# Kernel tuning notes

Measured on AMD Instinct MI355X. Metric: run time of the kernel, lower is better.

Reference implementation:

```python
import jax, jax.numpy as jnp
import numpy as np

N = 50000   # nodes
E = 600000  # edges / hyperedge incidences
D = 128     # node_in_dim
H = 128     # hidden_dim
TAU = 0.5
ALPHA = 0.5
LAM = 0.5

_PARAM_SHAPES = [('Wq0', (1, H)), ('bq0', (H,)), ('W0', (D, H)), ('b0', (H,)),
                 ('Whq0', (1, H)), ('bhq0', (H,)), ('Wh0', (D, H)), ('bh0', (H,)),
                 ('Wf0', (H, H)), ('bf0', (H,)), ('Wfh0', (H, H)), ('bfh0', (H,)),
                 ('aq0', (H,)), ('a0', (H,)), ('ahq0', (H,)), ('ah0', (H,)),
                 ('aq_', (H,)), ('a_', (H,)), ('ahq_', (H,)), ('ah_', (H,)),
                 ('Wlq', (1, H)), ('blq', (H,)), ('Wlf', (D, H)), ('blf', (H,)),
                 ('Wm1', (H, H)), ('bm1', (H,)), ('Wm2', (H, H)), ('bm2', (H,))]


def setup_inputs() -> dict:
    key = jax.random.key(0)
    ks = jax.random.split(key, 8 + len(_PARAM_SHAPES))
    inp = {}
    inp['feats'] = jax.random.normal(ks[0], (N, D), dtype=jnp.float32)
    inp['edge_index'] = jax.random.randint(ks[1], (2, E), 0, N).astype(jnp.int32)
    inp['edge_index_aug'] = jax.random.randint(ks[2], (2, E), 0, N).astype(jnp.int32)
    inp['pos'] = jax.random.randint(ks[3], (100,), 1, N).astype(jnp.int32)
    inp['q'] = 0
    for i, (nm, sh) in enumerate(_PARAM_SHAPES):
        inp[nm] = jax.random.normal(ks[4 + i], sh, dtype=jnp.float32) * 0.05
    return inp


def _forward(feats, Wq0, bq0, W0, b0, Whq0, bhq0, Wh0, bh0, Wf0, bf0, Wfh0, bfh0,
             aq0, a0, ahq0, ah0, aq_, a_, ahq_, ah_, Wlq, blq, Wlf, blf,
             Wm1, bm1, Wm2, bm2, edge_index, edge_index_aug, q, pos):
    # ---- GCNConv (PyG default: add self-loops + symmetric normalization) ----
    sl = jnp.arange(N, dtype=edge_index.dtype)
    src = jnp.concatenate([edge_index[0], sl])
    dst = jnp.concatenate([edge_index[1], sl])
    deg = jax.ops.segment_sum(jnp.ones(src.shape[0], jnp.float32), dst, num_segments=N)
    dinv = jax.lax.rsqrt(deg)  # deg >= 1 thanks to self-loops
    enorm = dinv[src] * dinv[dst]

    def gcn(x, W, b):
        xw = x @ W
        return jax.ops.segment_sum(xw[src] * enorm[:, None], dst, num_segments=N) + b

    # ---- HypergraphConv (PyG, no attention): X' = D^-1 H B^-1 H^T X W ----
    node = edge_index_aug[0]
    he = edge_index_aug[1]
    Be = jax.ops.segment_sum(jnp.ones((E,), jnp.float32), he, num_segments=N)
    Dn = jax.ops.segment_sum(jnp.ones((E,), jnp.float32), node, num_segments=N)
    Binv = jnp.where(Be > 0, 1.0 / Be, 0.0)
    Dninv = jnp.where(Dn > 0, 1.0 / Dn, 0.0)

    def hg(x, W, b):
        xw = x @ W
        me = jax.ops.segment_sum(xw[node], he, num_segments=N) * Binv[:, None]
        return jax.ops.segment_sum(me[he], node, num_segments=N) * Dninv[:, None] + b

    # ---- attention-weighted fusion of two views (softmax over 2 logits) ----
    def fuse(a, b, wa, wb):
        att = jax.nn.softmax(jnp.stack([a @ wa, b @ wb], axis=1), axis=1)  # [N,2]
        return att[:, 0:1] * a + att[:, 1:2] * b

    querys = jnp.zeros((N, 1), jnp.float32).at[q].set(1.0)
    hq = jax.nn.relu(gcn(querys, Wq0, bq0))
    h = jax.nn.relu(gcn(feats, W0, b0))
    hf = fuse(hq, h, aq0, a0)
    h_augq = jax.nn.relu(hg(querys, Whq0, bhq0))
    h_aug = jax.nn.relu(hg(feats, Wh0, bh0))
    h_augf = fuse(h_augq, h_aug, ahq0, ah0)
    querys2 = querys @ Wlq + blq
    feats2 = feats @ Wlf + blf
    hf_ = fuse(querys2, feats2, aq_, a_)
    hf = jax.nn.relu(hf + gcn(hf_, Wf0, bf0))
    hfh_ = fuse(querys2, feats2, ahq_, ah_)
    h_augf = jax.nn.relu(h_augf + hg(hfh_, Wfh0, bfh0))

    def mlp(x):
        return jax.nn.relu(x @ Wm1 + bm1) @ Wm2 + bm2

    z = mlp(hf)
    z_aug = mlp(h_augf)

    # ---- Contra loss ----
    def expcos(v, M):
        num = M @ v
        den = jnp.maximum(jnp.linalg.norm(M, axis=1) * jnp.linalg.norm(v), 1e-8)
        return jnp.exp(num / den / TAU)

    sim1 = expcos(z[q], z)
    sim_aug1 = expcos(z_aug[q], z_aug)
    sim2 = expcos(z[q], z_aug)
    sim_aug2 = expcos(z_aug[q], z)
    mask = jnp.zeros((N,), bool).at[pos].set(True).at[q].set(False)
    nmask = jnp.sum(mask).astype(jnp.float32)

    def nlm(s):  # mean over positives of -log(s_i / sum(s))
        r = jnp.log(jnp.sum(s)) - jnp.log(s)
        return jnp.sum(jnp.where(mask, r, 0.0)) / nmask

    loss_intra = 0.5 * (nlm(sim1) + nlm(sim_aug1))
    loss_inter = 0.5 * (nlm(sim2) + nlm(sim_aug2))
    z_unsup = jnp.log(jnp.sum(sim2)) - jnp.log(sim2[q])
    z_aug_unsup = jnp.log(jnp.sum(sim_aug2)) - jnp.log(sim_aug2[q])
    loss_unsup = 0.5 * z_unsup + 0.5 * z_aug_unsup
    return loss_intra + ALPHA * loss_inter + LAM * loss_unsup


def reference(feats, Wq0, bq0, W0, b0, Whq0, bhq0, Wh0, bh0, Wf0, bf0, Wfh0, bfh0,
              aq0, a0, ahq0, ah0, aq_, a_, ahq_, ah_, Wlq, blq, Wlf, blf,
              Wm1, bm1, Wm2, bm2, edge_index, edge_index_aug, q, pos):
    return _forward(feats, Wq0, bq0, W0, b0, Whq0, bhq0, Wh0, bh0, Wf0, bf0, Wfh0, bfh0,
                    aq0, a0, ahq0, ah0, aq_, a_, ahq_, ah_, Wlq, blq, Wlf, blf,
                    Wm1, bm1, Wm2, bm2, edge_index, edge_index_aug, q, pos)
```

## Files before the change

kernel.cpp:

```cpp
#include <hip/hip_runtime.h>

#define NN 50000
#define EE 600000
#define HH 128
#define TAU_INV 2.0f
#define PSZ 6250
#define CAP 48

#define BINB 512
#define BUFC 240
#define QCAP 80000
#define QPAD 16
#define WSUB 32
#define SUBN 196

typedef __attribute__((ext_vector_type(8))) short short8;
typedef __attribute__((ext_vector_type(4))) float f32x4;
typedef __attribute__((ext_vector_type(2))) float floatx2;

__device__ __forceinline__ float wsum64(float v) {
#pragma unroll
  for (int m = 32; m >= 1; m >>= 1) v += __shfl_xor(v, m, 64);
  return v;
}
__device__ __forceinline__ unsigned short f2bf(float f) {
  unsigned u = __builtin_bit_cast(unsigned, f);
  u = u + 0x7FFFu + ((u >> 16) & 1u);
  return (unsigned short)(u >> 16);
}
__device__ __forceinline__ float bf2f(unsigned short h) {
  unsigned u = ((unsigned)h) << 16;
  return __builtin_bit_cast(float, u);
}
__device__ __forceinline__ unsigned char fp8_enc1(float v) {
  int p = __builtin_amdgcn_cvt_pk_fp8_f32(v, v, 0, false);
  return (unsigned char)(p & 0xFF);
}
__device__ __forceinline__ void fp8x8_dec(uint2 v, float* f) {
  floatx2 a = __builtin_amdgcn_cvt_pk_f32_fp8(v.x, false);
  floatx2 b = __builtin_amdgcn_cvt_pk_f32_fp8(v.x, true);
  floatx2 c = __builtin_amdgcn_cvt_pk_f32_fp8(v.y, false);
  floatx2 d = __builtin_amdgcn_cvt_pk_f32_fp8(v.y, true);
  f[0] = a.x; f[1] = a.y; f[2] = b.x; f[3] = b.y;
  f[4] = c.x; f[5] = c.y; f[6] = d.x; f[7] = d.y;
}
__device__ __forceinline__ uint2 fp8x8_enc(const float* f) {
  int w0 = __builtin_amdgcn_cvt_pk_fp8_f32(f[0], f[1], 0, false);
  w0 = __builtin_amdgcn_cvt_pk_fp8_f32(f[2], f[3], w0, true);
  int w1 = __builtin_amdgcn_cvt_pk_fp8_f32(f[4], f[5], 0, false);
  w1 = __builtin_amdgcn_cvt_pk_fp8_f32(f[6], f[7], w1, true);
  return make_uint2((unsigned)w0, (unsigned)w1);
}

#define LDSW 136

__global__ __launch_bounds__(256) void bin_k(const int* __restrict__ ei,
                                             const int* __restrict__ ea,
                                             int* __restrict__ qcnt,
                                             unsigned int* __restrict__ qdata) {
  __shared__ int cnt[24], base[24], pfx[25];
  __shared__ unsigned int buf[24 * BUFC];
  const int tid = threadIdx.x;
  if (tid < 24) cnt[tid] = 0;
  __syncthreads();
  for (int e = blockIdx.x * 256 + tid; e < EE; e += BINB * 256) {
    int pay0 = __builtin_nontemporal_load(ei + e);
    int k0 = __builtin_nontemporal_load(ei + EE + e);
    int pay1 = __builtin_nontemporal_load(ea + e);
    int k1 = __builtin_nontemporal_load(ea + EE + e);
    int k2 = pay1, pay2 = k1;
    int g0 = k0 / PSZ;
    int g1 = 8 + k1 / PSZ;
    int g2 = 16 + k2 / PSZ;
    int o0 = atomicAdd(&cnt[g0], 1);
    int o1 = atomicAdd(&cnt[g1], 1);
    int o2 = atomicAdd(&cnt[g2], 1);
    if (o0 < BUFC) buf[g0 * BUFC + o0] = ((unsigned)k0 << 16) | (unsigned)pay0;
    if (o1 < BUFC) buf[g1 * BUFC + o1] = ((unsigned)k1 << 16) | (unsigned)pay1;
    if (o2 < BUFC) buf[g2 * BUFC + o2] = ((unsigned)k2 << 16) | (unsigned)pay2;
  }
  __syncthreads();
  if (tid < 24) {
    int c = min(cnt[tid], BUFC);
    cnt[tid] = c;
    base[tid] = atomicAdd(&qcnt[tid * QPAD], c);
  }
  __syncthreads();
  if (tid == 0) {
    int s = 0;
#pragma unroll
    for (int g = 0; g < 24; ++g) { pfx[g] = s; s += cnt[g]; }
    pfx[24] = s;
  }
  __syncthreads();
  const int total = pfx[24];
  for (int j = tid; j < total; j += 256) {
    int lo2 = 0, hi2 = 24;
    while (lo2 + 1 < hi2) {
      int mid = (lo2 + hi2) >> 1;
      if (j >= pfx[mid]) lo2 = mid; else hi2 = mid;
    }
    int g = lo2;
    int i = j - pfx[g];
    int dq = base[g] + i;
    if (dq < QCAP) qdata[(size_t)g * QCAP + dq] = buf[g * BUFC + i];
  }
}

__global__ __launch_bounds__(256) void fillp_k(const int* __restrict__ qcnt,
                                               const unsigned int* __restrict__ qdata,
                                               int* __restrict__ cursor,
                                               unsigned short* __restrict__ slotsA,
                                               unsigned short* __restrict__ slotsB,
                                               unsigned short* __restrict__ slotsC,
                                               float* __restrict__ cntq,
                                               const int* __restrict__ qp) {
  __shared__ int cur[SUBN];
  const int w = blockIdx.x;
  const int p = w & 7;
  const int r = (w >> 3) % 3;
  const int s = w / 24;
  const int lo = p * PSZ + s * SUBN;
  const int hi = min(lo + SUBN, (p + 1) * PSZ);
  const int tid = threadIdx.x;
  if (tid < SUBN) cur[tid] = 0;
  __syncthreads();
  const int g = r * 8 + p;
  const int qlen = min(qcnt[g * QPAD], QCAP);
  const unsigned int* qd = qdata + (size_t)g * QCAP;
  unsigned short* slots = (r == 0) ? slotsA : (r == 1) ? slotsB : slotsC;
  const int q = *qp;
  auto proc = [&](unsigned int rec) {
    int key = (int)(rec >> 16);
    if (key >= lo && key < hi) {
      int pay = (int)(rec & 0xFFFFu);
      int idx = atomicAdd(&cur[key - lo], 1);
      if (idx < CAP) slots[key * CAP + idx] = (unsigned short)pay;
      if (r == 1 && pay == q) atomicAdd(&cntq[key], 1.0f);
    }
  };
  const int nv4 = qlen >> 2;
  const uint4* qd4 = (const uint4*)qd;
  int j = tid;
  for (; j + 256 < nv4; j += 512) {
    uint4 r0 = qd4[j];
    uint4 r1 = qd4[j + 256];
    proc(r0.x); proc(r0.y); proc(r0.z); proc(r0.w);
    proc(r1.x); proc(r1.y); proc(r1.z); proc(r1.w);
  }
  if (j < nv4) {
    uint4 r0 = qd4[j];
    proc(r0.x); proc(r0.y); proc(r0.z); proc(r0.w);
  }
  int i = (nv4 << 2) + tid;
  if (i < qlen) proc(qd[i]);
  __syncthreads();
  for (int k = lo + tid; k < hi; k += 256) cursor[r * NN + k] = cur[k - lo];
}

__global__ void derive_k(const int* __restrict__ cursor, float* __restrict__ dinv,
                         float* __restrict__ Binv, float* __restrict__ Dninv,
                         const int* __restrict__ pos, const int* __restrict__ qp,
                         int* __restrict__ maskI) {
  int i = blockIdx.x * 256 + threadIdx.x;
  if (i < NN) {
    dinv[i] = rsqrtf((float)(cursor[i] + 1));
    int b = cursor[NN + i];
    Binv[i] = (b > 0) ? 1.0f / (float)b : 0.0f;
    int d = cursor[2 * NN + i];
    Dninv[i] = (d > 0) ? 1.0f / (float)d : 0.0f;
  }
  if (blockIdx.x == 0) {
    int t = threadIdx.x;
    if (t < 100) maskI[pos[t]] = 1;
    __syncthreads();
    if (t == 0) maskI[*qp] = 0;
  }
}

__device__ __forceinline__ void shq_body(const int* __restrict__ ei, const int* __restrict__ ea,
                                         const int* __restrict__ qp,
                                         const float* __restrict__ dinv,
                                         const float* __restrict__ Binv,
                                         const float* __restrict__ cntq,
                                         float* __restrict__ s_hq, float* __restrict__ s_hgq,
                                         int bid) {
  int e = bid * 256 + threadIdx.x;
  if (e >= EE) return;
  int q = *qp;
  int src = __builtin_nontemporal_load(ei + e);
  if (src == q) {
    int dst = __builtin_nontemporal_load(ei + EE + e);
    atomicAdd(&s_hq[dst], dinv[q] * dinv[dst]);
  }
  int he = __builtin_nontemporal_load(ea + EE + e);
  float cq = cntq[he];
  if (cq != 0.0f) {
    int node = __builtin_nontemporal_load(ea + e);
    atomicAdd(&s_hgq[node], Binv[he] * cq);
  }
  if (e == 0) atomicAdd(&s_hq[q], dinv[q] * dinv[q]);
}

__device__ __forceinline__ void fuse2_body(const unsigned short* __restrict__ f2,
                                           const int* __restrict__ qp,
                                           const float* __restrict__ Wlq,
                                           const float* __restrict__ blq,
                                           const float* __restrict__ aq1,
                                           const float* __restrict__ a1,
                                           const float* __restrict__ aq2,
                                           const float* __restrict__ a2,
                                           unsigned short* __restrict__ out1,
                                           unsigned short* __restrict__ out2, int bid) {
  int row = bid * 4 + (threadIdx.x >> 6);
  if (row >= NN) return;
  int lane = threadIdx.x & 63;
  int c0 = lane, c1 = lane + 64;
  int q = *qp;
  float q20 = blq[c0] + ((row == q) ? Wlq[c0] : 0.f);
  float q21 = blq[c1] + ((row == q) ? Wlq[c1] : 0.f);
  float f0 = bf2f(f2[(size_t)row * 128 + c0]);
  float f1 = bf2f(f2[(size_t)row * 128 + c1]);
  float dq1 = wsum64(q20 * aq1[c0] + q21 * aq1[c1]);
  float df1 = wsum64(f0 * a1[c0] + f1 * a1[c1]);
  float dq2 = wsum64(q20 * aq2[c0] + q21 * aq2[c1]);
  float df2 = wsum64(f0 * a2[c0] + f1 * a2[c1]);
  {
    float mx = fmaxf(dq1, df1);
    float e0 = expf(dq1 - mx), e1 = expf(df1 - mx);
    float w0 = e0 / (e0 + e1), w1 = 1.f - w0;
    out1[(size_t)row * 128 + c0] = f2bf(w0 * q20 + w1 * f0);
    out1[(size_t)row * 128 + c1] = f2bf(w0 * q21 + w1 * f1);
  }
  {
    float mx = fmaxf(dq2, df2);
    float e0 = expf(dq2 - mx), e1 = expf(df2 - mx);
    float w0 = e0 / (e0 + e1), w1 = 1.f - w0;
    out2[(size_t)row * 128 + c0] = f2bf(w0 * q20 + w1 * f0);
    out2[(size_t)row * 128 + c1] = f2bf(w0 * q21 + w1 * f1);
  }
}

__global__ __launch_bounds__(256) void f2_k(const int* __restrict__ ei,
                                            const int* __restrict__ ea,
                                            const int* __restrict__ qp,
                                            const float* __restrict__ dinv,
                                            const float* __restrict__ Binv,
                                            const float* __restrict__ cntq,
                                            float* __restrict__ s_hq,
                                            float* __restrict__ s_hgq,
                                            const unsigned short* __restrict__ B6,
                                            const float* __restrict__ Wlq,
                                            const float* __restrict__ blq,
                                            const float* __restrict__ aq_,
                                            const float* __restrict__ a_,
                                            const float* __restrict__ ahq_,
                                            const float* __restrict__ ah_,
                                            unsigned short* __restrict__ B3,
                                            unsigned short* __restrict__ B4, int eb) {
  int b = blockIdx.x;
  if (b < eb)
    shq_body(ei, ea, qp, dinv, Binv, cntq, s_hq, s_hgq, b);
  else
    fuse2_body(B6, qp, Wlq, blq, aq_, a_, ahq_, ah_, B3, B4, b - eb);
}

__global__ void pack_k(const float* __restrict__ W0, const float* __restrict__ Wh0,
                       const float* __restrict__ Wlf, const float* __restrict__ Wf0,
                       const float* __restrict__ Wfh0, const float* __restrict__ Wm1,
                       const float* __restrict__ Wm2, unsigned short* __restrict__ out) {
  int tid = blockIdx.x * 256 + threadIdx.x;
  if (tid >= 7 * 2048) return;
  int mat = tid >> 11, r = tid & 2047;
  int s = r >> 9, c = (r >> 6) & 7, lane = r & 63;
  const float* W = (mat == 0) ? W0 : (mat == 1) ? Wh0 : (mat == 2) ? Wlf
                 : (mat == 3) ? Wf0 : (mat == 4) ? Wfh0 : (mat == 5) ? Wm1 : Wm2;
  int k0 = 32 * s + (lane >> 4) * 8;
  int n = 16 * c + (lane & 15);
  unsigned short* o = out + (size_t)tid * 8;
#pragma unroll
  for (int j = 0; j < 8; ++j) o[j] = f2bf(W[(k0 + j) * 128 + n]);
}

template <bool BIAS, bool RELU, int OM>
__device__ __forceinline__ void gemm_core(unsigned short* As, const short8* Wp,
                                          const float* bias, void* outv, int r0, int nrows,
                                          int tid) {
  const int wave = tid >> 6, lane = tid & 63;
  const int quad = lane >> 4, l15 = lane & 15;
  f32x4 acc[8];
#pragma unroll
  for (int c = 0; c < 8; ++c) acc[c] = (f32x4){0.f, 0.f, 0.f, 0.f};
#pragma unroll
  for (int s = 0; s < 4; ++s) {
    short8 a = *(const short8*)&As[(wave * 16 + l15) * LDSW + s * 32 + quad * 8];
#pragma unroll
    for (int c = 0; c < 8; ++c) {
      short8 b = Wp[(s * 8 + c) * 64 + lane];
      acc[c] = __builtin_amdgcn_mfma_f32_16x16x32_bf16(a, b, acc[c], 0, 0, 0);
    }
  }
  __syncthreads();
  const int rwl = wave * 16 + quad * 4;
  if (OM == 2) {
    unsigned char* l8 = (unsigned char*)As;
#pragma unroll
    for (int c = 0; c < 8; ++c) {
      int col = c * 16 + l15;
      float bv = BIAS ? bias[col] : 0.f;
#pragma unroll
      for (int r = 0; r < 4; ++r) {
        float v = acc[c][r] + bv;
        if (RELU) v = fmaxf(v, 0.f);
        l8[(rwl + r) * 128 + col] = fp8_enc1(v);
      }
    }
    __syncthreads();
#pragma unroll
    for (int t = 0; t < 2; ++t) {
      int idx = (t * 256 + tid) * 16;
      int row = idx >> 7, off = idx & 127;
      int grow = r0 + row;
      if (grow < nrows)
        *(uint4*)&((unsigned char*)outv)[(size_t)grow * 256 + off] = *(uint4*)&l8[idx];
    }
  } else {
    unsigned short* l16 = As;
#pragma unroll
    for (int c = 0; c < 8; ++c) {
      int col = c * 16 + l15;
      float bv = BIAS ? bias[col] : 0.f;
#pragma unroll
      for (int r = 0; r < 4; ++r) {
        float v = acc[c][r] + bv;
        if (RELU) v = fmaxf(v, 0.f);
        l16[(rwl + r) * 128 + col] = f2bf(v);
      }
    }
    __syncthreads();
#pragma unroll
    for (int t = 0; t < 4; ++t) {
      int idx = (t * 256 + tid) * 16;
      int row = idx >> 8, off = idx & 255;
      int grow = r0 + row;
      if (grow < nrows)
        *(uint4*)&((unsigned char*)outv)[(size_t)grow * 256 + off] =
            *(uint4*)&((unsigned char*)l16)[idx];
    }
  }
}

__device__ __forceinline__ void stage_bf16(const unsigned short* A, unsigned short* As,
                                           int r0, int nrows, int tid) {
#pragma unroll
  for (int t = 0; t < 4; ++t) {
    int v = t * 256 + tid;
    int row = v >> 4, cc = v & 15;
    int gr = r0 + row;
    uint4 val = make_uint4(0, 0, 0, 0);
    if (gr < nrows) val = ((const uint4*)A)[(size_t)gr * 16 + cc];
    *(uint4*)&As[row * LDSW + cc * 8] = val;
  }
}

template <bool BIAS, bool RELU, int OM>
__global__ __launch_bounds__(256) void gemm2_mfma(const unsigned short* __restrict__ A0,
                                                  const unsigned short* __restrict__ A1,
                                                  const short8* __restrict__ Wp0,
                                                  const short8* __restrict__ Wp1,
                                                  const float* __restrict__ b0,
                                                  const float* __restrict__ b1,
                                                  void* __restrict__ o0, void* __restrict__ o1,
                                                  int nrows, int nblk) {
  __shared__ unsigned short As[64 * LDSW];
  int b = blockIdx.x;
  const unsigned short* A = A0;
  const short8* Wp = Wp0;
  const float* bias = b0;
  void* o = o0;
  if (b >= nblk) {
    b -= nblk; A = A1; Wp = Wp1; bias = b1; o = o1;
  }
  const int r0 = b * 64;
  stage_bf16(A, As, r0, nrows, threadIdx.x);
  __syncthreads();
  gemm_core<BIAS, RELU, OM>(As, Wp, bias, o, r0, nrows, threadIdx.x);
}

__global__ __launch_bounds__(256) void gemm3_mfma(const float* __restrict__ A,
                                                  const short8* __restrict__ Wp,
                                                  const float* __restrict__ bias2,
                                                  unsigned char* __restrict__ p1,
                                                  unsigned char* __restrict__ p2,
                                                  unsigned short* __restrict__ out2,
                                                  int nrows) {
  __shared__ unsigned short As[64 * LDSW];
  const int tid = threadIdx.x;
  const int bh = blockIdx.x & 1;
  const int r0 = (blockIdx.x >> 1) * 64;
#pragma unroll
  for (int t = 0; t < 8; ++t) {
    int v = t * 256 + tid;
    int row = v >> 5, c4 = v & 31;
    int gr = r0 + row;
    f32x4 val = (f32x4){0.f, 0.f, 0.f, 0.f};
    if (gr < nrows) val = ((const f32x4*)A)[(size_t)gr * 32 + c4];
    ushort4 o;
    o.x = f2bf(val.x); o.y = f2bf(val.y); o.z = f2bf(val.z); o.w = f2bf(val.w);
    *(ushort4*)&As[row * LDSW + c4 * 4] = o;
  }
  __syncthreads();
  const int wave = tid >> 6, lane = tid & 63;
  const int quad = lane >> 4, l15 = lane & 15;
  f32x4 acc[3][4];
#pragma unroll
  for (int m = 0; m < 3; ++m)
#pragma unroll
    for (int c = 0; c < 4; ++c) acc[m][c] = (f32x4){0.f, 0.f, 0.f, 0.f};
#pragma unroll
  for (int s = 0; s < 4; ++s) {
    short8 a = *(const short8*)&As[(wave * 16 + l15) * LDSW + s * 32 + quad * 8];
#pragma unroll
    for (int m = 0; m < 3; ++m)
#pragma unroll
      for (int c = 0; c < 4; ++c) {
        short8 bb = Wp[(size_t)m * 2048 + (s * 8 + bh * 4 + c) * 64 + lane];
        acc[m][c] = __builtin_amdgcn_mfma_f32_16x16x32_bf16(a, bb, acc[m][c], 0, 0, 0);
      }
  }
  __syncthreads();
  unsigned char* l8a = (unsigned char*)As;
  unsigned char* l8b = l8a + 4096;
  unsigned short* l16 = (unsigned short*)(l8a + 8192);
  const int rwl = wave * 16 + quad * 4;
#pragma unroll
  for (int c = 0; c < 4; ++c) {
    int coll = c * 16 + l15;
    float bv = bias2[(bh * 4 + c) * 16 + l15];
#pragma unroll
    for (int r = 0; r < 4; ++r) {
      int lrow = rwl + r;
      l8a[lrow * 64 + coll] = fp8_enc1(acc[0][c][r]);
      l8b[lrow * 64 + coll] = fp8_enc1(acc[1][c][r]);
      l16[lrow * 64 + coll] = f2bf(acc[2][c][r] + bv);
    }
  }
  __syncthreads();
  {
    int idx = tid * 16;
    int row = idx >> 6, off = idx & 63;
    int grow = r0 + row;
    if (grow < nrows) {
      *(uint4*)&p1[(size_t)grow * 256 + bh * 64 + off] = *(uint4*)&l8a[idx];
      *(uint4*)&p2[(size_t)grow * 256 + bh * 64 + off] = *(uint4*)&l8b[idx];
    }
  }
#pragma unroll
  for (int t = 0; t < 2; ++t) {
    int idx = (t * 256 + tid) * 16;
    int row = idx >> 7, off = idx & 127;
    int grow = r0 + row;
    if (grow < nrows)
      *(uint4*)&((unsigned char*)out2)[(size_t)grow * 256 + bh * 128 + off] =
          *(uint4*)&((unsigned char*)l16)[idx];
  }
}

template <int MODE, bool OUTFP8>
__device__ __forceinline__ void gpair_body(const uint2* __restrict__ xp,
                                           unsigned short* __restrict__ y1,
                                           unsigned short* __restrict__ y2,
                                           uint2* __restrict__ yp,
                                           const int* __restrict__ cnt,
                                           const unsigned short* __restrict__ slots,
                                           const float* __restrict__ wv, int blk) {
  int node = blk * 8 + (threadIdx.x >> 5);
  if (node >= NN) return;
  int l = threadIdx.x & 31;
  int st = node * CAP;
  int n = min(cnt[node], CAP);
  float acc[8];
#pragma unroll
  for (int i = 0; i < 8; ++i) acc[i] = 0.f;
  int p = 0;
  for (; p + 4 <= n; p += 4) {
    ushort4 s4 = *(const ushort4*)&slots[st + p];
    uint2 v0 = xp[(size_t)s4.x * 32 + l];
    uint2 v1 = xp[(size_t)s4.y * 32 + l];
    uint2 v2 = xp[(size_t)s4.z * 32 + l];
    uint2 v3 = xp[(size_t)s4.w * 32 + l];
    float f[8];
    if (MODE == 0) {
      float w0 = wv[s4.x], w1 = wv[s4.y], w2 = wv[s4.z], w3 = wv[s4.w];
      fp8x8_dec(v0, f);
#pragma unroll
      for (int i = 0; i < 8; ++i) acc[i] = fmaf(w0, f[i], acc[i]);
      fp8x8_dec(v1, f);
#pragma unroll
      for (int i = 0; i < 8; ++i) acc[i] = fmaf(w1, f[i], acc[i]);
      fp8x8_dec(v2, f);
#pragma unroll
      for (int i = 0; i < 8; ++i) acc[i] = fmaf(w2, f[i], acc[i]);
      fp8x8_dec(v3, f);
#pragma unroll
      for (int i = 0; i < 8; ++i) acc[i] = fmaf(w3, f[i], acc[i]);
    } else {
      fp8x8_dec(v0, f);
#pragma unroll
      for (int i = 0; i < 8; ++i) acc[i] += f[i];
      fp8x8_dec(v1, f);
#pragma unroll
      for (int i = 0; i < 8; ++i) acc[i] += f[i];
      fp8x8_dec(v2, f);
#pragma unroll
      for (int i = 0; i < 8; ++i) acc[i] += f[i];
      fp8x8_dec(v3, f);
#pragma unroll
      for (int i = 0; i < 8; ++i) acc[i] += f[i];
    }
  }
  for (; p < n; ++p) {
    int s = slots[st + p];
    uint2 v = xp[(size_t)s * 32 + l];
    float f[8];
    fp8x8_dec(v, f);
    if (MODE == 0) {
      float w = wv[s];
#pragma unroll
      for (int i = 0; i < 8; ++i) acc[i] = fmaf(w, f[i], acc[i]);
    } else {
#pragma unroll
      for (int i = 0; i < 8; ++i) acc[i] += f[i];
    }
  }
  float sc = wv[node];
  if (MODE == 0) {
    uint2 v = xp[(size_t)node * 32 + l];
    float f[8];
    fp8x8_dec(v, f);
#pragma unroll
    for (int i = 0; i < 8; ++i) acc[i] = sc * fmaf(sc, f[i], acc[i]);
  } else {
#pragma unroll
    for (int i = 0; i < 8; ++i) acc[i] *= sc;
  }
  if (OUTFP8) {
    yp[(size_t)node * 32 + l] = fp8x8_enc(acc);
  } else {
    unsigned short* y = (l < 16) ? y1 : y2;
    int cg = l & 15;
    uint4 o;
    o.x = ((unsigned)f2bf(acc[1]) << 16) | f2bf(acc[0]);
    o.y = ((unsigned)f2bf(acc[3]) << 16) | f2bf(acc[2]);
    o.z = ((unsigned)f2bf(acc[5]) << 16) | f2bf(acc[4]);
    o.w = ((unsigned)f2bf(acc[7]) << 16) | f2bf(acc[6]);
    *(uint4*)&y[(size_t)node * 128 + cg * 8] = o;
  }
}

__global__ void dgather12_k(const uint2* __restrict__ xp1, unsigned short* __restrict__ y1a,
                            unsigned short* __restrict__ y1b, const uint2* __restrict__ xp2,
                            uint2* __restrict__ yp3, const int* __restrict__ cursor,
                            const unsigned short* __restrict__ slotsA,
                            const unsigned short* __restrict__ slotsB,
                            const float* __restrict__ dinv, const float* __restrict__ Binv,
                            int nblk) {
  int b = blockIdx.x;
  if (b < nblk)
    gpair_body<0, false>(xp1, y1a, y1b, nullptr, cursor, slotsA, dinv, b);
  else
    gpair_body<1, true>(xp2, nullptr, nullptr, yp3, cursor + NN, slotsB, Binv, b - nblk);
}

__global__ void dgather3_k(const uint2* __restrict__ xp, unsigned short* __restrict__ y1,
                           unsigned short* __restrict__ y2, const int* __restrict__ cursor,
                           const unsigned short* __restrict__ slotsC,
                           const float* __restrict__ wv) {
  gpair_body<1, false>(xp, y1, y2, nullptr, cursor + 2 * NN, slotsC, wv, blockIdx.x);
}

__device__ __forceinline__ void fuse_add_body(const unsigned short* __restrict__ g,
                                              const unsigned short* __restrict__ gr,
                                              const float* __restrict__ svec,
                                              const float* __restrict__ dscale,
                                              const float* __restrict__ Wq,
                                              const float* __restrict__ bq,
                                              const float* __restrict__ bm,
                                              const float* __restrict__ aq,
                                              const float* __restrict__ am,
                                              const float* __restrict__ bres,
                                              unsigned short* __restrict__ out, int blk) {
  int row = blk * 4 + (threadIdx.x >> 6);
  if (row >= NN) return;
  int lane = threadIdx.x & 63;
  int c0 = lane, c1 = lane + 64;
  float s = svec[row];
  if (dscale) s *= dscale[row];
  float hq0 = fmaxf(fmaf(s, Wq[c0], bq[c0]), 0.f);
  float hq1 = fmaxf(fmaf(s, Wq[c1], bq[c1]), 0.f);
  float h0 = fmaxf(bf2f(g[(size_t)row * 128 + c0]) + bm[c0], 0.f);
  float h1 = fmaxf(bf2f(g[(size_t)row * 128 + c1]) + bm[c1], 0.f);
  float dq = wsum64(hq0 * aq[c0] + hq1 * aq[c1]);
  float dm = wsum64(h0 * am[c0] + h1 * am[c1]);
  float mx = fmaxf(dq, dm);
  float e0 = expf(dq - mx), e1 = expf(dm - mx);
  float w0 = e0 / (e0 + e1), w1 = 1.f - w0;
  float r0 = fmaxf(w0 * hq0 + w1 * h0 + bf2f(gr[(size_t)row * 128 + c0]) + bres[c0], 0.f);
  float r1 = fmaxf(w0 * hq1 + w1 * h1 + bf2f(gr[(size_t)row * 128 + c1]) + bres[c1], 0.f);
  out[(size_t)row * 128 + c0] = f2bf(r0);
  out[(size_t)row * 128 + c1] = f2bf(r1);
}

__global__ void fuse_add2_k(const unsigned short* gA, const unsigned short* grA,
                            const float* svA, const float* dsA, const float* WqA,
                            const float* bqA, const float* bmA, const float* aqA,
                            const float* amA, const float* brA, unsigned short* outA,
                            const unsigned short* gB, const unsigned short* grB,
                            const float* svB, const float* dsB, const float* WqB,
                            const float* bqB, const float* bmB, const float* aqB,
                            const float* amB, const float* brB, unsigned short* outB,
                            int nblk) {
  int b = blockIdx.x;
  if (b < nblk)
    fuse_add_body(gA, grA, svA, dsA, WqA, bqA, bmA, aqA, amA, brA, outA, b);
  else
    fuse_add_body(gB, grB, svB, dsB, WqB, bqB, bmB, aqB, amB, brB, outB, b - nblk);
}

__global__ void sim_k(const unsigned short* __restrict__ z,
                      const unsigned short* __restrict__ za, const int* __restrict__ qp,
                      float4* __restrict__ simbuf, float* __restrict__ scal_out) {
  int row = blockIdx.x * 4 + (threadIdx.x >> 6);
  if (row >= NN) return;
  int lane = threadIdx.x & 63;
  int c0 = lane, c1 = lane + 64;
  int q = *qp;
  float zi0 = bf2f(z[(size_t)row * 128 + c0]), zi1 = bf2f(z[(size_t)row * 128 + c1]);
  float zai0 = bf2f(za[(size_t)row * 128 + c0]), zai1 = bf2f(za[(size_t)row * 128 + c1]);
  float zq0 = bf2f(z[(size_t)q * 128 + c0]), zq1 = bf2f(z[(size_t)q * 128 + c1]);
  float zaq0 = bf2f(za[(size_t)q * 128 + c0]), zaq1 = bf2f(za[(size_t)q * 128 + c1]);
  float nzi = wsum64(zi0 * zi0 + zi1 * zi1);
  float nzai = wsum64(zai0 * zai0 + zai1 * zai1);
  float nzq = wsum64(zq0 * zq0 + zq1 * zq1);
  float nzaq = wsum64(zaq0 * zaq0 + zaq1 * zaq1);
  float d1 = wsum64(zi0 * zq0 + zi1 * zq1);
  float d2 = wsum64(zai0 * zaq0 + zai1 * zaq1);
  float d3 = wsum64(zai0 * zq0 + zai1 * zq1);
  float d4 = wsum64(zi0 * zaq0 + zi1 * zaq1);
  if (lane == 0) {
    float ni = sqrtf(nzi), nai = sqrtf(nzai);
    float nq = sqrtf(nzq), naq = sqrtf(nzaq);
    float c1_ = d1 / fmaxf(ni * nq, 1e-8f) * TAU_INV;
    float ca1 = d2 / fmaxf(nai * naq, 1e-8f) * TAU_INV;
    float c2_ = d3 / fmaxf(nai * nq, 1e-8f) * TAU_INV;
    float ca2 = d4 / fmaxf(ni * naq, 1e-8f) * TAU_INV;
    simbuf[row] = make_float4(c1_, ca1, c2_, ca2);
    if (row == q) {
      scal_out[9] = c2_;
      scal_out[10] = ca2;
    }
  }
}

__global__ __launch_bounds__(256) void reduce_sim_k(const float4* __restrict__ simbuf,
                                                    const int* __restrict__ maskI,
                                                    float* __restrict__ scal) {
  float acc[9];
#pragma unroll
  for (int i = 0; i < 9; ++i) acc[i] = 0.f;
  for (int row = blockIdx.x * 256 + threadIdx.x; row < NN; row += gridDim.x * 256) {
    float4 v = simbuf[row];
    acc[0] += expf(v.x);
    acc[1] += expf(v.y);
    acc[2] += expf(v.z);
    acc[3] += expf(v.w);
    if (maskI[row]) {
      acc[4] += v.x; acc[5] += v.y; acc[6] += v.z; acc[7] += v.w;
      acc[8] += 1.0f;
    }
  }
  __shared__ float s[9][4];
  int lane = threadIdx.x & 63, wv = threadIdx.x >> 6;
#pragma unroll
  for (int i = 0; i < 9; ++i) {
    float r = wsum64(acc[i]);
    if (lane == 0) s[i][wv] = r;
  }
  __syncthreads();
  if (threadIdx.x < 9) {
    float r = s[threadIdx.x][0] + s[threadIdx.x][1] + s[threadIdx.x][2] + s[threadIdx.x][3];
    atomicAdd(&scal[threadIdx.x], r);
  }
}

__global__ void final_k(const float* __restrict__ scal, float* __restrict__ out) {
  if (threadIdx.x != 0 || blockIdx.x != 0) return;
  float S1 = scal[0], Sa1 = scal[1], S2 = scal[2], Sa2 = scal[3];
  float L1 = scal[4], La1 = scal[5], L2 = scal[6], La2 = scal[7];
  float NM = scal[8], Q2 = scal[9], Qa2 = scal[10];
  float intra = 0.5f * ((logf(S1) - L1 / NM) + (logf(Sa1) - La1 / NM));
  float inter = 0.5f * ((logf(S2) - L2 / NM) + (logf(Sa2) - La2 / NM));
  float unsup = 0.5f * (logf(S2) - Q2) + 0.5f * (logf(Sa2) - Qa2);
  out[0] = intra + 0.5f * inter + 0.5f * unsup;
}

extern "C" void kernel_launch(void* const* d_in, const int* in_sizes, int n_in,
                              void* d_out, int out_size, void* d_ws, size_t ws_size,
                              hipStream_t stream) {
  const float* feats = (const float*)d_in[0];
  const int* ei = (const int*)d_in[1];
  const int* ea = (const int*)d_in[2];
  const int* pos = (const int*)d_in[3];
  const int* qp = (const int*)d_in[4];
  const float* Wq0 = (const float*)d_in[5];
  const float* bq0 = (const float*)d_in[6];
  const float* W0 = (const float*)d_in[7];
  const float* b0 = (const float*)d_in[8];
  const float* Whq0 = (const float*)d_in[9];
  const float* bhq0 = (const float*)d_in[10];
  const float* Wh0 = (const float*)d_in[11];
  const float* bh0 = (const float*)d_in[12];
  const float* Wf0 = (const float*)d_in[13];
  const float* bf0 = (const float*)d_in[14];
  const float* Wfh0 = (const float*)d_in[15];
  const float* bfh0 = (const float*)d_in[16];
  const float* aq0 = (const float*)d_in[17];
  const float* a0 = (const float*)d_in[18];
  const float* ahq0 = (const float*)d_in[19];
  const float* ah0 = (const float*)d_in[20];
  const float* aq_ = (const float*)d_in[21];
  const float* a_ = (const float*)d_in[22];
  const float* ahq_ = (const float*)d_in[23];
  const float* ah_ = (const float*)d_in[24];
  const float* Wlq = (const float*)d_in[25];
  const float* blq = (const float*)d_in[26];
  const float* Wlf = (const float*)d_in[27];
  const float* blf = (const float*)d_in[28];
  const float* Wm1 = (const float*)d_in[29];
  const float* bm1 = (const float*)d_in[30];
  const float* Wm2 = (const float*)d_in[31];
  const float* bm2 = (const float*)d_in[32];

  char* ws = (char*)d_ws;
  size_t off = 0;
  auto take = [&](size_t bytes) -> void* {
    void* p = ws + off;
    off = (off + bytes + 255) & ~(size_t)255;
    return p;
  };
  int* cursor3 = (int*)take(3 * NN * 4);
  int* maskI = (int*)take(NN * 4);
  float* s_hq = (float*)take(NN * 4);
  float* cntq = (float*)take(NN * 4);
  float* s_hgq = (float*)take(NN * 4);
  float* scal = (float*)take(64 * 4);
  int* qcnt = (int*)take(24 * QPAD * 4);
  size_t zero_end = off;
  unsigned short* slotsA = (unsigned short*)take((size_t)NN * CAP * 2);
  unsigned short* slotsB = (unsigned short*)take((size_t)NN * CAP * 2);
  unsigned short* slotsC = (unsigned short*)take((size_t)NN * CAP * 2);
  unsigned int* qdata = (unsigned int*)take((size_t)24 * QCAP * 4);
  float* dinv = (float*)take(NN * 4);
  float* Binv = (float*)take(NN * 4);
  float* Dninv = (float*)take(NN * 4);
  float4* simbuf = (float4*)take((size_t)NN * 16);
  unsigned short* Wpack = (unsigned short*)take((size_t)7 * 16384 * 2);
  const size_t BFSZ = (size_t)NN * HH * 2;
  unsigned short* B0 = (unsigned short*)take(BFSZ);
  unsigned short* B1 = (unsigned short*)take(BFSZ);
  unsigned short* B2 = (unsigned short*)take(BFSZ);
  unsigned short* B3 = (unsigned short*)take(BFSZ);
  unsigned short* B4 = (unsigned short*)take(BFSZ);
  unsigned short* B5 = (unsigned short*)take(BFSZ);
  unsigned short* B6 = (unsigned short*)take(BFSZ);
  unsigned char* P1 = (unsigned char*)take((size_t)NN * 256);
  unsigned char* P2 = (unsigned char*)take((size_t)NN * 256);
  unsigned char* P3 = (unsigned char*)take((size_t)NN * 256);

  const int NB = (NN + 255) / 256;
  const int EB = (EE + 255) / 256;
  const int GMB = (NN + 63) / 64;
  const int GTB = (NN + 7) / 8;
  const int RB = (NN + 3) / 4;
  const short8* Wp = (const short8*)Wpack;

  hipMemsetAsync(d_ws, 0, zero_end, stream);
  pack_k<<<(7 * 2048 + 255) / 256, 256, 0, stream>>>(W0, Wh0, Wlf, Wf0, Wfh0, Wm1, Wm2,
                                                     Wpack);
  bin_k<<<BINB, 256, 0, stream>>>(ei, ea, qcnt, qdata);
  fillp_k<<<24 * WSUB, 256, 0, stream>>>(qcnt, qdata, cursor3, slotsA, slotsB, slotsC,
                                         cntq, qp);
  gemm3_mfma<<<2 * GMB, 256, 0, stream>>>(feats, Wp, blf, P1, P2, B6, NN);
  derive_k<<<NB, 256, 0, stream>>>(cursor3, dinv, Binv, Dninv, pos, qp, maskI);
  f2_k<<<EB + RB, 256, 0, stream>>>(ei, ea, qp, dinv, Binv, cntq, s_hq, s_hgq, B6, Wlq,
                                    blq, aq_, a_, ahq_, ah_, B3, B4, EB);
  gemm2_mfma<false, false, 2><<<2 * GMB, 256, 0, stream>>>(
      B3, B4, Wp + (size_t)3 * 2048, Wp + (size_t)4 * 2048, nullptr, nullptr, P1 + 128,
      P2 + 128, NN, GMB);
  dgather12_k<<<2 * GTB, 256, 0, stream>>>((const uint2*)P1, B0, B1, (const uint2*)P2,
                                           (uint2*)P3, cursor3, slotsA, slotsB, dinv, Binv,
                                           GTB);
  dgather3_k<<<GTB, 256, 0, stream>>>((const uint2*)P3, B2, B5, cursor3, slotsC, Dninv);
  fuse_add2_k<<<2 * RB, 256, 0, stream>>>(
      B0, B1, s_hq, nullptr, Wq0, bq0, b0, aq0, a0, bf0, B3,
      B2, B5, s_hgq, Dninv, Whq0, bhq0, bh0, ahq0, ah0, bfh0, B4, RB);
  gemm2_mfma<true, true, 1><<<2 * GMB, 256, 0, stream>>>(
      B3, B4, Wp + (size_t)5 * 2048, Wp + (size_t)5 * 2048, bm1, bm1, B0, B1, NN, GMB);
  gemm2_mfma<true, false, 1><<<2 * GMB, 256, 0, stream>>>(
      B0, B1, Wp + (size_t)6 * 2048, Wp + (size_t)6 * 2048, bm2, bm2, B2, B5, NN, GMB);
  sim_k<<<RB, 256, 0, stream>>>(B2, B5, qp, simbuf, scal);
  reduce_sim_k<<<64, 256, 0, stream>>>(simbuf, maskI, scal);
  final_k<<<1, 64, 0, stream>>>(scal, (float*)d_out);
}
```

Baseline: 426.4 us.

## Split gather neighbor lists across half-waves and fold derive kernel into fill

The gather kernels now give each node a full 64-lane wave instead of 32 lanes. The two half-waves take alternating neighbor slots and their partial sums are combined with a cross-half shuffle, which doubles the memory-level parallelism per node on the irregular fp8 gathers. Separately, the derive_k launch is removed: degree inverses are computed in fillp_k as the counts are written, and the mask setup moves into bin_k. This saves one launch and a reread of the cursor array, at the cost of twice as many blocks and one more shuffle reduction in the gather kernels.

```diff
diff --git a/kernel.cpp b/kernel.cpp
--- a/kernel.cpp
+++ b/kernel.cpp
@@ -57,12 +57,17 @@
 __global__ __launch_bounds__(256) void bin_k(const int* __restrict__ ei,
                                              const int* __restrict__ ea,
                                              int* __restrict__ qcnt,
-                                             unsigned int* __restrict__ qdata) {
+                                             unsigned int* __restrict__ qdata,
+                                             const int* __restrict__ pos,
+                                             const int* __restrict__ qp,
+                                             int* __restrict__ maskI) {
   __shared__ int cnt[24], base[24], pfx[25];
   __shared__ unsigned int buf[24 * BUFC];
   const int tid = threadIdx.x;
   if (tid < 24) cnt[tid] = 0;
-  __syncthreads();
+  if (blockIdx.x == 0 && tid < 100) maskI[pos[tid]] = 1;
+  __syncthreads();
+  if (blockIdx.x == 0 && tid == 0) maskI[*qp] = 0;
   for (int e = blockIdx.x * 256 + tid; e < EE; e += BINB * 256) {
     int pay0 = __builtin_nontemporal_load(ei + e);
     int k0 = __builtin_nontemporal_load(ei + EE + e);
@@ -114,7 +119,10 @@
                                                unsigned short* __restrict__ slotsB,
                                                unsigned short* __restrict__ slotsC,
                                                float* __restrict__ cntq,
-                                               const int* __restrict__ qp) {
+                                               const int* __restrict__ qp,
+                                               float* __restrict__ dinv,
+                                               float* __restrict__ Binv,
+                                               float* __restrict__ Dninv) {
   __shared__ int cur[SUBN];
   const int w = blockIdx.x;
   const int p = w & 7;
@@ -155,26 +163,12 @@
   int i = (nv4 << 2) + tid;
   if (i < qlen) proc(qd[i]);
   __syncthreads();
-  for (int k = lo + tid; k < hi; k += 256) cursor[r * NN + k] = cur[k - lo];
-}
-
-__global__ void derive_k(const int* __restrict__ cursor, float* __restrict__ dinv,
-                         float* __restrict__ Binv, float* __restrict__ Dninv,
-                         const int* __restrict__ pos, const int* __restrict__ qp,
-                         int* __restrict__ maskI) {
-  int i = blockIdx.x * 256 + threadIdx.x;
-  if (i < NN) {
-    dinv[i] = rsqrtf((float)(cursor[i] + 1));
-    int b = cursor[NN + i];
-    Binv[i] = (b > 0) ? 1.0f / (float)b : 0.0f;
-    int d = cursor[2 * NN + i];
-    Dninv[i] = (d > 0) ? 1.0f / (float)d : 0.0f;
-  }
-  if (blockIdx.x == 0) {
-    int t = threadIdx.x;
-    if (t < 100) maskI[pos[t]] = 1;
-    __syncthreads();
-    if (t == 0) maskI[*qp] = 0;
+  for (int k = lo + tid; k < hi; k += 256) {
+    int c = cur[k - lo];
+    cursor[r * NN + k] = c;
+    if (r == 0) dinv[k] = rsqrtf((float)(c + 1));
+    else if (r == 1) Binv[k] = (c > 0) ? 1.0f / (float)c : 0.0f;
+    else Dninv[k] = (c > 0) ? 1.0f / (float)c : 0.0f;
   }
 }
 
@@ -474,24 +468,29 @@
                                            const int* __restrict__ cnt,
                                            const unsigned short* __restrict__ slots,
                                            const float* __restrict__ wv, int blk) {
-  int node = blk * 8 + (threadIdx.x >> 5);
+  int node = blk * 4 + (threadIdx.x >> 6);
   if (node >= NN) return;
-  int l = threadIdx.x & 31;
-  int st = node * CAP;
-  int n = min(cnt[node], CAP);
+  const int lane = threadIdx.x & 63;
+  const int l = lane & 31;
+  const int h = lane >> 5;
+  const int st = node * CAP;
+  const int n = min(cnt[node], CAP);
   float acc[8];
 #pragma unroll
   for (int i = 0; i < 8; ++i) acc[i] = 0.f;
-  int p = 0;
-  for (; p + 4 <= n; p += 4) {
-    ushort4 s4 = *(const ushort4*)&slots[st + p];
-    uint2 v0 = xp[(size_t)s4.x * 32 + l];
-    uint2 v1 = xp[(size_t)s4.y * 32 + l];
-    uint2 v2 = xp[(size_t)s4.z * 32 + l];
-    uint2 v3 = xp[(size_t)s4.w * 32 + l];
+  int j = h;
+  for (; j + 6 < n; j += 8) {
+    int s0 = slots[st + j];
+    int s1 = slots[st + j + 2];
+    int s2 = slots[st + j + 4];
+    int s3 = slots[st + j + 6];
+    uint2 v0 = xp[(size_t)s0 * 32 + l];
+    uint2 v1 = xp[(size_t)s1 * 32 + l];
+    uint2 v2 = xp[(size_t)s2 * 32 + l];
+    uint2 v3 = xp[(size_t)s3 * 32 + l];
     float f[8];
     if (MODE == 0) {
-      float w0 = wv[s4.x], w1 = wv[s4.y], w2 = wv[s4.z], w3 = wv[s4.w];
+      float w0 = wv[s0], w1 = wv[s1], w2 = wv[s2], w3 = wv[s3];
       fp8x8_dec(v0, f);
 #pragma unroll
       for (int i = 0; i < 8; ++i) acc[i] = fmaf(w0, f[i], acc[i]);
@@ -519,20 +518,45 @@
       for (int i = 0; i < 8; ++i) acc[i] += f[i];
     }
   }
-  for (; p < n; ++p) {
-    int s = slots[st + p];
-    uint2 v = xp[(size_t)s * 32 + l];
+  for (; j + 2 < n; j += 4) {
+    int s0 = slots[st + j];
+    int s1 = slots[st + j + 2];
+    uint2 v0 = xp[(size_t)s0 * 32 + l];
+    uint2 v1 = xp[(size_t)s1 * 32 + l];
     float f[8];
-    fp8x8_dec(v, f);
     if (MODE == 0) {
-      float w = wv[s];
-#pragma unroll
-      for (int i = 0; i < 8; ++i) acc[i] = fmaf(w, f[i], acc[i]);
+      float w0 = wv[s0], w1 = wv[s1];
+      fp8x8_dec(v0, f);
+#pragma unroll
+      for (int i = 0; i < 8; ++i) acc[i] = fmaf(w0, f[i], acc[i]);
+      fp8x8_dec(v1, f);
+#pragma unroll
+      for (int i = 0; i < 8; ++i) acc[i] = fmaf(w1, f[i], acc[i]);
     } else {
+      fp8x8_dec(v0, f);
 #pragma unroll
       for (int i = 0; i < 8; ++i) acc[i] += f[i];
-    }
-  }
+      fp8x8_dec(v1, f);
+#pragma unroll
+      for (int i = 0; i < 8; ++i) acc[i] += f[i];
+    }
+  }
+  if (j < n) {
+    int s0 = slots[st + j];
+    uint2 v0 = xp[(size_t)s0 * 32 + l];
+    float f[8];
+    fp8x8_dec(v0, f);
+    if (MODE == 0) {
+      float w0 = wv[s0];
+#pragma unroll
+      for (int i = 0; i < 8; ++i) acc[i] = fmaf(w0, f[i], acc[i]);
+    } else {
+#pragma unroll
+      for (int i = 0; i < 8; ++i) acc[i] += f[i];
+    }
+  }
+#pragma unroll
+  for (int i = 0; i < 8; ++i) acc[i] += __shfl_xor(acc[i], 32, 64);
   float sc = wv[node];
   if (MODE == 0) {
     uint2 v = xp[(size_t)node * 32 + l];
@@ -544,17 +568,19 @@
 #pragma unroll
     for (int i = 0; i < 8; ++i) acc[i] *= sc;
   }
-  if (OUTFP8) {
-    yp[(size_t)node * 32 + l] = fp8x8_enc(acc);
-  } else {
-    unsigned short* y = (l < 16) ? y1 : y2;
-    int cg = l & 15;
-    uint4 o;
-    o.x = ((unsigned)f2bf(acc[1]) << 16) | f2bf(acc[0]);
-    o.y = ((unsigned)f2bf(acc[3]) << 16) | f2bf(acc[2]);
-    o.z = ((unsigned)f2bf(acc[5]) << 16) | f2bf(acc[4]);
-    o.w = ((unsigned)f2bf(acc[7]) << 16) | f2bf(acc[6]);
-    *(uint4*)&y[(size_t)node * 128 + cg * 8] = o;
+  if (h == 0) {
+    if (OUTFP8) {
+      yp[(size_t)node * 32 + l] = fp8x8_enc(acc);
+    } else {
+      unsigned short* y = (l < 16) ? y1 : y2;
+      int cg = l & 15;
+      uint4 o;
+      o.x = ((unsigned)f2bf(acc[1]) << 16) | f2bf(acc[0]);
+      o.y = ((unsigned)f2bf(acc[3]) << 16) | f2bf(acc[2]);
+      o.z = ((unsigned)f2bf(acc[5]) << 16) | f2bf(acc[4]);
+      o.w = ((unsigned)f2bf(acc[7]) << 16) | f2bf(acc[6]);
+      *(uint4*)&y[(size_t)node * 128 + cg * 8] = o;
+    }
   }
 }
 
@@ -777,30 +803,28 @@
   unsigned char* P2 = (unsigned char*)take((size_t)NN * 256);
   unsigned char* P3 = (unsigned char*)take((size_t)NN * 256);
 
-  const int NB = (NN + 255) / 256;
   const int EB = (EE + 255) / 256;
   const int GMB = (NN + 63) / 64;
-  const int GTB = (NN + 7) / 8;
+  const int GT4 = (NN + 3) / 4;
   const int RB = (NN + 3) / 4;
   const short8* Wp = (const short8*)Wpack;
 
   hipMemsetAsync(d_ws, 0, zero_end, stream);
   pack_k<<<(7 * 2048 + 255) / 256, 256, 0, stream>>>(W0, Wh0, Wlf, Wf0, Wfh0, Wm1, Wm2,
                                                      Wpack);
-  bin_k<<<BINB, 256, 0, stream>>>(ei, ea, qcnt, qdata);
+  bin_k<<<BINB, 256, 0, stream>>>(ei, ea, qcnt, qdata, pos, qp, maskI);
   fillp_k<<<24 * WSUB, 256, 0, stream>>>(qcnt, qdata, cursor3, slotsA, slotsB, slotsC,
-                                         cntq, qp);
+                                         cntq, qp, dinv, Binv, Dninv);
   gemm3_mfma<<<2 * GMB, 256, 0, stream>>>(feats, Wp, blf, P1, P2, B6, NN);
-  derive_k<<<NB, 256, 0, stream>>>(cursor3, dinv, Binv, Dninv, pos, qp, maskI);
   f2_k<<<EB + RB, 256, 0, stream>>>(ei, ea, qp, dinv, Binv, cntq, s_hq, s_hgq, B6, Wlq,
                                     blq, aq_, a_, ahq_, ah_, B3, B4, EB);
   gemm2_mfma<false, false, 2><<<2 * GMB, 256, 0, stream>>>(
       B3, B4, Wp + (size_t)3 * 2048, Wp + (size_t)4 * 2048, nullptr, nullptr, P1 + 128,
       P2 + 128, NN, GMB);
-  dgather12_k<<<2 * GTB, 256, 0, stream>>>((const uint2*)P1, B0, B1, (const uint2*)P2,
+  dgather12_k<<<2 * GT4, 256, 0, stream>>>((const uint2*)P1, B0, B1, (const uint2*)P2,
                                            (uint2*)P3, cursor3, slotsA, slotsB, dinv, Binv,
-                                           GTB);
-  dgather3_k<<<GTB, 256, 0, stream>>>((const uint2*)P3, B2, B5, cursor3, slotsC, Dninv);
+                                           GT4);
+  dgather3_k<<<GT4, 256, 0, stream>>>((const uint2*)P3, B2, B5, cursor3, slotsC, Dninv);
   fuse_add2_k<<<2 * RB, 256, 0, stream>>>(
       B0, B1, s_hq, nullptr, Wq0, bq0, b0, aq0, a0, bf0, B3,
       B2, B5, s_hgq, Dninv, Whq0, bhq0, bh0, ahq0, ah0, bfh0, B4, RB);
```

Result: no change. 430.0 us (+0.8%).
